# Kernel optimization log

Hardware: AMD Instinct MI355X
Metric: run time of the kernel (lower is better)

Reference implementation:

```python
import jax, jax.numpy as jnp
import numpy as np

N_HEAD = 12
EPS_NORM = 1e-12   # F.normalize eps
EPS_DENOM = 1e-6   # clamp(min=1e-6)


def _l2norm(t):
    n = jnp.sqrt(jnp.sum(t * t, axis=-1, keepdims=True))
    return t / jnp.maximum(n, EPS_NORM)


def setup_inputs() -> dict:
    key = jax.random.key(0)
    ks = jax.random.split(key, 5)
    B, T, C = 1, 4096, 768
    x = jax.random.normal(ks[0], (B, T, C), dtype=jnp.float32)
    w_attn = jax.random.normal(ks[1], (C, 3 * C), dtype=jnp.float32) * 0.02
    b_attn = jnp.zeros((3 * C,), dtype=jnp.float32)
    w_proj = jax.random.normal(ks[2], (C, C), dtype=jnp.float32) * 0.02
    b_proj = jnp.zeros((C,), dtype=jnp.float32)
    return {"x": x, "w_attn": w_attn, "b_attn": b_attn,
            "w_proj": w_proj, "b_proj": b_proj}


def reference(x, w_attn, b_attn, w_proj, b_proj):
    B, T, C = x.shape
    H = N_HEAD
    hd = C // H
    qkv = x @ w_attn + b_attn                      # [B,T,3C]
    q, k, v = jnp.split(qkv, 3, axis=-1)
    # [B,T,C] -> [B,H,T,hd]
    def to_heads(t):
        return t.reshape(B, T, H, hd).transpose(0, 2, 1, 3)
    q, k, v = to_heads(q), to_heads(k), to_heads(v)
    # T > 512 branch: normalized-qk cumulative linear attention
    q = _l2norm(q)
    k = _l2norm(k)
    num = jnp.einsum('bhqd,bhkd->bhqk', q, k)      # [B,H,T,T]
    denom = jnp.maximum(jnp.cumsum(num, axis=-1), EPS_DENOM)
    att = num / denom
    y = jnp.einsum('bhqk,bhkd->bhqd', att, v)      # [B,H,T,hd]
    y = y.transpose(0, 2, 1, 3).reshape(B, T, C)
    return y @ w_proj + b_proj
```

## Files before the change

kernel.cpp:

```cpp
#include <hip/hip_runtime.h>

#define T_SEQ 4096
#define H_NUM 12
#define HD    64
#define C_DIM 768
#define N_QKV 2304
#define HT    (T_SEQ * HD)
#define KT_TOT (T_SEQ / 64)

typedef float    f32x4 __attribute__((ext_vector_type(4)));
typedef float    f32x2 __attribute__((ext_vector_type(2)));
typedef _Float16 half8 __attribute__((ext_vector_type(8)));
typedef _Float16 half4 __attribute__((ext_vector_type(4)));
typedef _Float16 half2v __attribute__((ext_vector_type(2)));
typedef __fp16   fp16x2 __attribute__((ext_vector_type(2)));
typedef unsigned uint4v __attribute__((ext_vector_type(4)));

#define GLDS(gp, lp) __builtin_amdgcn_global_load_lds( \
    (const __attribute__((address_space(1))) void*)(gp), \
    (__attribute__((address_space(3))) void*)(lp), 16, 0, 0)

__device__ __forceinline__ void permlane32_swap(unsigned& a, unsigned& b) {
    asm("v_permlane32_swap_b32 %0, %1" : "+v"(a), "+v"(b));
}
__device__ __forceinline__ void permlane16_swap(unsigned& a, unsigned& b) {
    asm("v_permlane16_swap_b32 %0, %1" : "+v"(a), "+v"(b));
}

__global__ __launch_bounds__(256) void split_x_kernel(
    const float* __restrict__ x, _Float16* __restrict__ xh,
    _Float16* __restrict__ xl, int n4)
{
    const int i = blockIdx.x * 256 + threadIdx.x;
    if (i >= n4) return;
    const float4 v = ((const float4*)x)[i];
    const float vv[4] = {v.x, v.y, v.z, v.w};
    half4 h, l;
    #pragma unroll
    for (int j = 0; j < 4; ++j) {
        const _Float16 hh = (_Float16)vv[j];
        h[j] = hh;
        l[j] = (_Float16)(vv[j] - (float)hh);
    }
    ((half4*)xh)[i] = h;
    ((half4*)xl)[i] = l;
}

__global__ __launch_bounds__(256) void split_wt_kernel(
    const float* __restrict__ W, _Float16* __restrict__ wth,
    _Float16* __restrict__ wtl)
{
    __shared__ float Ws[64][65];
    const int tid = threadIdx.x;
    const int n0 = blockIdx.x * 64, k0 = blockIdx.y * 64;
    const int lr = tid >> 4, lc = (tid & 15) << 2;
    #pragma unroll
    for (int i = 0; i < 4; ++i) {
        const float4 v = *(const float4*)(W + (size_t)(k0 + lr + i * 16) * N_QKV + n0 + lc);
        Ws[lr + i * 16][lc + 0] = v.x; Ws[lr + i * 16][lc + 1] = v.y;
        Ws[lr + i * 16][lc + 2] = v.z; Ws[lr + i * 16][lc + 3] = v.w;
    }
    __syncthreads();
    const int n = tid >> 2, ks = (tid & 3) << 4;
    half8 h0, h1, l0, l1;
    #pragma unroll
    for (int j = 0; j < 8; ++j) {
        const float v = Ws[ks + j][n];
        const _Float16 hh = (_Float16)v;
        h0[j] = hh; l0[j] = (_Float16)(v - (float)hh);
    }
    #pragma unroll
    for (int j = 0; j < 8; ++j) {
        const float v = Ws[ks + 8 + j][n];
        const _Float16 hh = (_Float16)v;
        h1[j] = hh; l1[j] = (_Float16)(v - (float)hh);
    }
    const size_t dst = (size_t)(n0 + n) * C_DIM + k0 + ks;
    *(half8*)(wth + dst) = h0; *(half8*)(wth + dst + 8) = h1;
    *(half8*)(wtl + dst) = l0; *(half8*)(wtl + dst + 8) = l1;
}

__global__ __launch_bounds__(256) void gemm_qkv_kernel(
    const _Float16* __restrict__ xh, const _Float16* __restrict__ xl,
    const _Float16* __restrict__ wth, const _Float16* __restrict__ wtl,
    const float* __restrict__ bias,
    _Float16* __restrict__ qhi, _Float16* __restrict__ qlo,
    _Float16* __restrict__ khi, _Float16* __restrict__ klo,
    _Float16* __restrict__ vt)
{
    __shared__ __align__(16) _Float16 AH[128 * 64];
    __shared__ __align__(16) _Float16 AL[128 * 64];
    __shared__ __align__(16) _Float16 BH[64 * 64];
    __shared__ __align__(16) _Float16 BL[64 * 64];
    const int tid = threadIdx.x;
    const int wv = tid >> 6, lane = tid & 63;
    const int fm = lane & 15, fg = lane >> 4;
    const int lrow = lane >> 3;
    const int lcs  = (lane & 7) ^ (lrow & 7);
    const int bx = blockIdx.x;
    const int m0 = blockIdx.y * 128;

    auto dma_chunk = [&](int c) {
        const int kc0 = c * 64;
        #pragma unroll
        for (int i = 0; i < 12; ++i) {
            const int qidx = wv * 12 + i;
            if (qidx < 16) {
                const int rg = qidx;
                GLDS(xh + (size_t)(m0 + rg * 8 + lrow) * C_DIM + kc0 + lcs * 8, &AH[rg * 512]);
            } else if (qidx < 32) {
                const int rg = qidx - 16;
                GLDS(xl + (size_t)(m0 + rg * 8 + lrow) * C_DIM + kc0 + lcs * 8, &AL[rg * 512]);
            } else if (qidx < 40) {
                const int rg = qidx - 32;
                GLDS(wth + (size_t)(bx * 64 + rg * 8 + lrow) * C_DIM + kc0 + lcs * 8, &BH[rg * 512]);
            } else {
                const int rg = qidx - 40;
                GLDS(wtl + (size_t)(bx * 64 + rg * 8 + lrow) * C_DIM + kc0 + lcs * 8, &BL[rg * 512]);
            }
        }
    };

    f32x4 acc[2][4];
    #pragma unroll
    for (int mt = 0; mt < 2; ++mt)
        #pragma unroll
        for (int ct = 0; ct < 4; ++ct) acc[mt][ct] = (f32x4){0.f, 0.f, 0.f, 0.f};

    const int swz = fm & 7;
    dma_chunk(0);
    #pragma unroll 1
    for (int c = 0; c < C_DIM / 64; ++c) {
        __syncthreads();
        half8 ah[2][2], al[2][2], bh[4][2], bl[4][2];
        #pragma unroll
        for (int mt = 0; mt < 2; ++mt) {
            const int rb = (wv * 32 + mt * 16 + fm) * 64;
            #pragma unroll
            for (int kc = 0; kc < 2; ++kc) {
                const int cb = ((kc * 4 + fg) ^ swz) * 8;
                ah[mt][kc] = *(const half8*)&AH[rb + cb];
                al[mt][kc] = *(const half8*)&AL[rb + cb];
            }
        }
        #pragma unroll
        for (int ct = 0; ct < 4; ++ct) {
            const int rb = (ct * 16 + fm) * 64;
            #pragma unroll
            for (int kc = 0; kc < 2; ++kc) {
                const int cb = ((kc * 4 + fg) ^ swz) * 8;
                bh[ct][kc] = *(const half8*)&BH[rb + cb];
                bl[ct][kc] = *(const half8*)&BL[rb + cb];
            }
        }
        __syncthreads();
        if (c + 1 < C_DIM / 64) dma_chunk(c + 1);
        #pragma unroll
        for (int mt = 0; mt < 2; ++mt)
            #pragma unroll
            for (int ct = 0; ct < 4; ++ct)
                #pragma unroll
                for (int kc = 0; kc < 2; ++kc) {
                    acc[mt][ct] = __builtin_amdgcn_mfma_f32_16x16x32_f16(ah[mt][kc], bh[ct][kc], acc[mt][ct], 0, 0, 0);
                    acc[mt][ct] = __builtin_amdgcn_mfma_f32_16x16x32_f16(ah[mt][kc], bl[ct][kc], acc[mt][ct], 0, 0, 0);
                    acc[mt][ct] = __builtin_amdgcn_mfma_f32_16x16x32_f16(al[mt][kc], bh[ct][kc], acc[mt][ct], 0, 0, 0);
                }
    }

    const int sec = bx / 12, h = bx % 12;
    const size_t hb = (size_t)h * HT;
    float bb[4];
    #pragma unroll
    for (int ct = 0; ct < 4; ++ct) bb[ct] = bias[bx * 64 + ct * 16 + fm];

    if (sec < 2) {
        _Float16* dh = (sec == 0) ? qhi : khi;
        _Float16* dl = (sec == 0) ? qlo : klo;
        #pragma unroll
        for (int mt = 0; mt < 2; ++mt)
            #pragma unroll
            for (int r = 0; r < 4; ++r) {
                float o[4];
                float ss = 0.f;
                #pragma unroll
                for (int ct = 0; ct < 4; ++ct) {
                    o[ct] = acc[mt][ct][r] + bb[ct];
                    ss += o[ct] * o[ct];
                }
                #pragma unroll
                for (int mk = 1; mk < 16; mk <<= 1) ss += __shfl_xor(ss, mk, 16);
                const float invn = 1.0f / fmaxf(sqrtf(ss), 1e-12f);
                const int t = m0 + wv * 32 + mt * 16 + fg * 4 + r;
                const size_t rb = hb + (size_t)t * HD;
                #pragma unroll
                for (int ct = 0; ct < 4; ++ct) {
                    const float v = o[ct] * invn;
                    const _Float16 vh = (_Float16)v;
                    dh[rb + ct * 16 + fm] = vh;
                    dl[rb + ct * 16 + fm] = (_Float16)(v - (float)vh);
                }
            }
    } else {
        #pragma unroll
        for (int mt = 0; mt < 2; ++mt) {
            const int t0 = m0 + wv * 32 + mt * 16 + fg * 4;
            #pragma unroll
            for (int ct = 0; ct < 4; ++ct) {
                half4 pk;
                #pragma unroll
                for (int r = 0; r < 4; ++r) pk[r] = (_Float16)(acc[mt][ct][r] + bb[ct]);
                *(half4*)(vt + hb + (size_t)(ct * 16 + fm) * T_SEQ + t0) = pk;
            }
        }
    }
}

__global__ __launch_bounds__(256) void attn_kernel(
    const _Float16* __restrict__ qhi, const _Float16* __restrict__ qlo,
    const _Float16* __restrict__ khi, const _Float16* __restrict__ klo,
    const _Float16* __restrict__ vt,  _Float16* __restrict__ ylin)
{
    __shared__ __align__(16) _Float16 KH[2][64 * 64];
    __shared__ __align__(16) _Float16 KL[2][64 * 64];
    __shared__ __align__(16) _Float16 VS[2][64 * 64];

    const int tid = threadIdx.x;
    const int wv = tid >> 6, lane = tid & 63;
    const int fm = lane & 15, fg = lane >> 4;
    const int lrow = lane >> 3;
    const int lcs  = (lane & 7) ^ (lrow & 7);
    const int h = blockIdx.y, qt = blockIdx.x;
    const size_t hb = (size_t)h * HT;

    const int q = qt * 64 + wv * 16 + fm;
    half8 qf[2][2];
    #pragma unroll
    for (int kc = 0; kc < 2; ++kc) {
        const size_t off = hb + (size_t)q * HD + kc * 32 + fg * 8;
        qf[0][kc] = *(const half8*)(qhi + off);
        qf[1][kc] = *(const half8*)(qlo + off);
    }

    const _Float16* ga[6];
    _Float16*       lb[6];
    int             gstr[6];
    #pragma unroll
    for (int i = 0; i < 6; ++i) {
        const int qidx = wv * 6 + i;
        const int rg = qidx & 7;
        if (qidx < 8) {
            ga[i] = khi + hb + (size_t)(rg * 8 + lrow) * HD + lcs * 8;
            lb[i] = &KH[0][rg * 512];
            gstr[i] = 64 * HD;
        } else if (qidx < 16) {
            ga[i] = klo + hb + (size_t)(rg * 8 + lrow) * HD + lcs * 8;
            lb[i] = &KL[0][rg * 512];
            gstr[i] = 64 * HD;
        } else {
            ga[i] = vt + hb + (size_t)(rg * 8 + lrow) * T_SEQ + lcs * 8;
            lb[i] = &VS[0][rg * 512];
            gstr[i] = 64;
        }
    }
    auto issue_tiles = [&](int bufoff) {
        #pragma unroll
        for (int i = 0; i < 6; ++i) {
            GLDS(ga[i], lb[i] + bufoff);
            ga[i] += gstr[i];
        }
    };

    f32x4 yacc[4];
    #pragma unroll
    for (int ct = 0; ct < 4; ++ct) yacc[ct] = (f32x4){0.f, 0.f, 0.f, 0.f};
    float carry = 0.0f;
    const int swz = fm & 7;

    issue_tiles(0);
    #pragma unroll 1
    for (int kt = 0; kt < KT_TOT; ++kt) {
        const int cur = kt & 1;
        __syncthreads();
        if (kt + 1 < KT_TOT) issue_tiles((cur ^ 1) * 4096);

        half8 ka[4][2], kl[4][2], vf[4][2];
        #pragma unroll
        for (int kr = 0; kr < 4; ++kr) {
            const int rb = (kr * 16 + fm) * 64;
            #pragma unroll
            for (int kc = 0; kc < 2; ++kc) {
                const int cb = ((kc * 4 + fg) ^ swz) * 8;
                ka[kr][kc] = *(const half8*)&KH[cur][rb + cb];
                kl[kr][kc] = *(const half8*)&KL[cur][rb + cb];
            }
        }
        #pragma unroll
        for (int ct = 0; ct < 4; ++ct) {
            const int rb = (ct * 16 + fm) * 64;
            #pragma unroll
            for (int kc = 0; kc < 2; ++kc)
                vf[ct][kc] = *(const half8*)&VS[cur][rb + (((kc * 4 + fg) ^ swz) * 8)];
        }

        f32x4 sacc[4];
        #pragma unroll
        for (int kr = 0; kr < 4; ++kr) sacc[kr] = (f32x4){0.f, 0.f, 0.f, 0.f};
        #pragma unroll
        for (int kr = 0; kr < 4; ++kr)
            #pragma unroll
            for (int kc = 0; kc < 2; ++kc) {
                sacc[kr] = __builtin_amdgcn_mfma_f32_16x16x32_f16(ka[kr][kc], qf[0][kc], sacc[kr], 0, 0, 0);
                sacc[kr] = __builtin_amdgcn_mfma_f32_16x16x32_f16(ka[kr][kc], qf[1][kc], sacc[kr], 0, 0, 0);
                sacc[kr] = __builtin_amdgcn_mfma_f32_16x16x32_f16(kl[kr][kc], qf[0][kc], sacc[kr], 0, 0, 0);
            }

        unsigned pk[4][2];
        #pragma unroll
        for (int pr = 0; pr < 2; ++pr) {
            const int kra = 2 * pr, krb = 2 * pr + 1;
            const f32x2 S0 = {sacc[kra][0], sacc[krb][0]};
            const f32x2 S1 = {sacc[kra][1], sacc[krb][1]};
            const f32x2 S2 = {sacc[kra][2], sacc[krb][2]};
            const f32x2 S3 = {sacc[kra][3], sacc[krb][3]};
            const f32x2 P1 = S0 + S1;
            const f32x2 P2 = P1 + S2;
            const f32x2 P3 = P2 + S3;
            f32x2 U1;
            U1[0] = __shfl_xor(P3[0], 16, 64);
            U1[1] = __shfl_xor(P3[1], 16, 64);
            const f32x2 PAIR = P3 + U1;
            f32x2 U2;
            U2[0] = __shfl_xor(PAIR[0], 32, 64);
            U2[1] = __shfl_xor(PAIR[1], 32, 64);
            const f32x2 TOT = PAIR + U2;
            #pragma unroll
            for (int qq = 0; qq < 2; ++qq) {
                const int kr = 2 * pr + qq;
                const float pref = ((fg & 1) ? U1[qq] : 0.0f) + ((fg & 2) ? U2[qq] : 0.0f);
                const float base = carry + pref;
                carry += TOT[qq];
                const f32x2 b2 = {base, base};
                const f32x2 d01 = b2 + (f32x2){S0[qq], P1[qq]};
                const f32x2 d23 = b2 + (f32x2){P2[qq], P3[qq]};
                const f32x2 eps = {1e-6f, 1e-6f};
                const f32x2 m01 = __builtin_elementwise_max(d01, eps);
                const f32x2 m23 = __builtin_elementwise_max(d23, eps);
                const f32x2 r01 = {__builtin_amdgcn_rcpf(m01[0]), __builtin_amdgcn_rcpf(m01[1])};
                const f32x2 r23 = {__builtin_amdgcn_rcpf(m23[0]), __builtin_amdgcn_rcpf(m23[1])};
                const f32x2 n01 = {S0[qq], S1[qq]};
                const f32x2 n23 = {S2[qq], S3[qq]};
                const f32x2 sc = {0.03125f, 0.03125f};
                const f32x2 a01 = (n01 * r01) * sc;
                const f32x2 a23 = (n23 * r23) * sc;
                const fp16x2 c0 = __builtin_amdgcn_cvt_pkrtz(a01[0], a01[1]);
                const fp16x2 c1 = __builtin_amdgcn_cvt_pkrtz(a23[0], a23[1]);
                pk[kr][0] = __builtin_bit_cast(unsigned, c0);
                pk[kr][1] = __builtin_bit_cast(unsigned, c1);
            }
        }

        #pragma unroll
        for (int g = 0; g < 2; ++g)
            #pragma unroll
            for (int hh = 0; hh < 2; ++hh) {
                permlane32_swap(pk[g * 2 + 0][hh], pk[g * 2 + 1][hh]);
                permlane16_swap(pk[g * 2 + 0][hh], pk[g * 2 + 1][hh]);
            }

        #pragma unroll
        for (int kc = 0; kc < 2; ++kc) {
            const uint4v u = {pk[2 * kc][0], pk[2 * kc][1],
                              pk[2 * kc + 1][0], pk[2 * kc + 1][1]};
            const half8 af = __builtin_bit_cast(half8, u);
            #pragma unroll
            for (int ct = 0; ct < 4; ++ct)
                yacc[ct] = __builtin_amdgcn_mfma_f32_16x16x32_f16(af, vf[ct][kc], yacc[ct], 0, 0, 0);
        }
    }

    #pragma unroll
    for (int ct = 0; ct < 4; ++ct)
        #pragma unroll
        for (int r = 0; r < 4; ++r) {
            const int t = qt * 64 + wv * 16 + fg * 4 + r;
            ylin[(size_t)t * C_DIM + h * HD + ct * 16 + fm] =
                (_Float16)(yacc[ct][r] * 0.0078125f);
        }
}

__global__ __launch_bounds__(256) void gemm_proj_kernel(
    const _Float16* __restrict__ A, const float* __restrict__ W,
    const float* __restrict__ bias, float* __restrict__ out)
{
    __shared__ _Float16 As[64][72];
    __shared__ _Float16 Bt[64][72];
    const int tid = threadIdx.x;
    const int w = tid >> 6, lane = tid & 63;
    const int m = lane & 15, g = lane >> 4;
    const int row0 = blockIdx.x << 6, col0 = blockIdx.y << 6;
    const int ar = tid >> 3, ac8 = (tid & 7) << 3;
    const int bn0 = (tid & 15) << 2, bpv = tid >> 4;
    f32x4 acc[4];
    #pragma unroll
    for (int ct = 0; ct < 4; ++ct) acc[ct] = (f32x4){0.f, 0.f, 0.f, 0.f};

    for (int kt = 0; kt < C_DIM; kt += 64) {
        half8 av0 = *(const half8*)(A + (size_t)(row0 + ar)      * C_DIM + kt + ac8);
        half8 av1 = *(const half8*)(A + (size_t)(row0 + ar + 32) * C_DIM + kt + ac8);
        float4 w0[2], w1[2];
        #pragma unroll
        for (int i = 0; i < 2; ++i) {
            const int k = kt + 2 * (bpv + 16 * i);
            w0[i] = *(const float4*)(W + (size_t)k       * C_DIM + col0 + bn0);
            w1[i] = *(const float4*)(W + (size_t)(k + 1) * C_DIM + col0 + bn0);
        }
        __syncthreads();
        *(half8*)&As[ar][ac8]      = av0;
        *(half8*)&As[ar + 32][ac8] = av1;
        #pragma unroll
        for (int i = 0; i < 2; ++i) {
            const int p = bpv + 16 * i;
            const float a_[4] = {w0[i].x, w0[i].y, w0[i].z, w0[i].w};
            const float b_[4] = {w1[i].x, w1[i].y, w1[i].z, w1[i].w};
            #pragma unroll
            for (int u = 0; u < 4; ++u) {
                half2v pk = {(_Float16)a_[u], (_Float16)b_[u]};
                *(half2v*)&Bt[bn0 + u][2 * p] = pk;
            }
        }
        __syncthreads();
        #pragma unroll
        for (int kc = 0; kc < 2; ++kc) {
            const half8 a = *(half8*)&As[w * 16 + m][kc * 32 + g * 8];
            #pragma unroll
            for (int ct = 0; ct < 4; ++ct) {
                const half8 b = *(half8*)&Bt[ct * 16 + m][kc * 32 + g * 8];
                acc[ct] = __builtin_amdgcn_mfma_f32_16x16x32_f16(a, b, acc[ct], 0, 0, 0);
            }
        }
    }
    #pragma unroll
    for (int ct = 0; ct < 4; ++ct)
        #pragma unroll
        for (int r = 0; r < 4; ++r) {
            const int t = row0 + w * 16 + g * 4 + r;
            const int n = col0 + ct * 16 + m;
            out[(size_t)t * C_DIM + n] = acc[ct][r] * 4096.0f + bias[n];
        }
}

extern "C" void kernel_launch(void* const* d_in, const int* in_sizes, int n_in,
                              void* d_out, int out_size, void* d_ws, size_t ws_size,
                              hipStream_t stream)
{
    const float* x      = (const float*)d_in[0];
    const float* w_attn = (const float*)d_in[1];
    const float* b_attn = (const float*)d_in[2];
    const float* w_proj = (const float*)d_in[3];
    const float* b_proj = (const float*)d_in[4];
    float* out = (float*)d_out;

    const size_t perQK = (size_t)H_NUM * HT;
    const size_t perX  = (size_t)T_SEQ * C_DIM;
    const size_t perW  = (size_t)N_QKV * C_DIM;
    _Float16* base = (_Float16*)d_ws;
    _Float16* xhi  = base;
    _Float16* xlo  = xhi + perX;
    _Float16* wthi = xlo + perX;
    _Float16* wtlo = wthi + perW;
    _Float16* qhi  = wtlo + perW;
    _Float16* qlo  = qhi + perQK;
    _Float16* khi  = qlo + perQK;
    _Float16* klo  = khi + perQK;
    _Float16* vtp  = klo + perQK;
    _Float16* ylin = xhi;

    split_x_kernel<<<(perX / 4 + 255) / 256, 256, 0, stream>>>(x, xhi, xlo, perX / 4);
    split_wt_kernel<<<dim3(N_QKV / 64, C_DIM / 64), 256, 0, stream>>>(w_attn, wthi, wtlo);
    gemm_qkv_kernel<<<dim3(N_QKV / 64, T_SEQ / 128), 256, 0, stream>>>(
        xhi, xlo, wthi, wtlo, b_attn, qhi, qlo, khi, klo, vtp);
    attn_kernel<<<dim3(T_SEQ / 64, H_NUM), 256, 0, stream>>>(
        qhi, qlo, khi, klo, vtp, ylin);
    gemm_proj_kernel<<<dim3(T_SEQ / 64, C_DIM / 64), 256, 0, stream>>>(
        ylin, w_proj, b_proj, out);
}
```

Measured before the change: 302.2 us.

## Software-pipeline QK^T of next tile with scan and PV of current tile

After: 321.0 us. 6.2% more time.

```diff
diff --git a/kernel.cpp b/kernel.cpp
--- a/kernel.cpp
+++ b/kernel.cpp
@@ -276,52 +276,49 @@
     float carry = 0.0f;
     const int swz = fm & 7;
 
-    issue_tiles(0);
-    #pragma unroll 1
-    for (int kt = 0; kt < KT_TOT; ++kt) {
-        const int cur = kt & 1;
-        __syncthreads();
-        if (kt + 1 < KT_TOT) issue_tiles((cur ^ 1) * 4096);
-
-        half8 ka[4][2], kl[4][2], vf[4][2];
+    f32x4 saccA[4], saccB[4];
+    half8 vfA[4][2], vfB[4][2];
+
+    auto qkt = [&](int nb, f32x4 (&sn)[4]) {
         #pragma unroll
         for (int kr = 0; kr < 4; ++kr) {
             const int rb = (kr * 16 + fm) * 64;
-            #pragma unroll
-            for (int kc = 0; kc < 2; ++kc) {
-                const int cb = ((kc * 4 + fg) ^ swz) * 8;
-                ka[kr][kc] = *(const half8*)&KH[cur][rb + cb];
-                kl[kr][kc] = *(const half8*)&KL[cur][rb + cb];
-            }
-        }
+            const int cb0 = (fg ^ swz) * 8;
+            const int cb1 = ((4 + fg) ^ swz) * 8;
+            const half8 a0 = *(const half8*)&KH[nb][rb + cb0];
+            const half8 a1 = *(const half8*)&KH[nb][rb + cb1];
+            const half8 l0 = *(const half8*)&KL[nb][rb + cb0];
+            const half8 l1 = *(const half8*)&KL[nb][rb + cb1];
+            f32x4 s = (f32x4){0.f, 0.f, 0.f, 0.f};
+            s = __builtin_amdgcn_mfma_f32_16x16x32_f16(a0, qf[0][0], s, 0, 0, 0);
+            s = __builtin_amdgcn_mfma_f32_16x16x32_f16(a0, qf[1][0], s, 0, 0, 0);
+            s = __builtin_amdgcn_mfma_f32_16x16x32_f16(l0, qf[0][0], s, 0, 0, 0);
+            s = __builtin_amdgcn_mfma_f32_16x16x32_f16(a1, qf[0][1], s, 0, 0, 0);
+            s = __builtin_amdgcn_mfma_f32_16x16x32_f16(a1, qf[1][1], s, 0, 0, 0);
+            s = __builtin_amdgcn_mfma_f32_16x16x32_f16(l1, qf[0][1], s, 0, 0, 0);
+            sn[kr] = s;
+        }
+    };
+
+    auto rdv = [&](int nb, half8 (&v)[4][2]) {
         #pragma unroll
         for (int ct = 0; ct < 4; ++ct) {
             const int rb = (ct * 16 + fm) * 64;
             #pragma unroll
             for (int kc = 0; kc < 2; ++kc)
-                vf[ct][kc] = *(const half8*)&VS[cur][rb + (((kc * 4 + fg) ^ swz) * 8)];
-        }
-
-        f32x4 sacc[4];
-        #pragma unroll
-        for (int kr = 0; kr < 4; ++kr) sacc[kr] = (f32x4){0.f, 0.f, 0.f, 0.f};
-        #pragma unroll
-        for (int kr = 0; kr < 4; ++kr)
-            #pragma unroll
-            for (int kc = 0; kc < 2; ++kc) {
-                sacc[kr] = __builtin_amdgcn_mfma_f32_16x16x32_f16(ka[kr][kc], qf[0][kc], sacc[kr], 0, 0, 0);
-                sacc[kr] = __builtin_amdgcn_mfma_f32_16x16x32_f16(ka[kr][kc], qf[1][kc], sacc[kr], 0, 0, 0);
-                sacc[kr] = __builtin_amdgcn_mfma_f32_16x16x32_f16(kl[kr][kc], qf[0][kc], sacc[kr], 0, 0, 0);
-            }
-
+                v[ct][kc] = *(const half8*)&VS[nb][rb + (((kc * 4 + fg) ^ swz) * 8)];
+        }
+    };
+
+    auto scanpv = [&](f32x4 (&s)[4], half8 (&v)[4][2]) {
         unsigned pk[4][2];
         #pragma unroll
         for (int pr = 0; pr < 2; ++pr) {
             const int kra = 2 * pr, krb = 2 * pr + 1;
-            const f32x2 S0 = {sacc[kra][0], sacc[krb][0]};
-            const f32x2 S1 = {sacc[kra][1], sacc[krb][1]};
-            const f32x2 S2 = {sacc[kra][2], sacc[krb][2]};
-            const f32x2 S3 = {sacc[kra][3], sacc[krb][3]};
+            const f32x2 S0 = {s[kra][0], s[krb][0]};
+            const f32x2 S1 = {s[kra][1], s[krb][1]};
+            const f32x2 S2 = {s[kra][2], s[krb][2]};
+            const f32x2 S3 = {s[kra][3], s[krb][3]};
             const f32x2 P1 = S0 + S1;
             const f32x2 P2 = P1 + S2;
             const f32x2 P3 = P2 + S3;
@@ -358,7 +355,6 @@
                 pk[kr][1] = __builtin_bit_cast(unsigned, c1);
             }
         }
-
         #pragma unroll
         for (int g = 0; g < 2; ++g)
             #pragma unroll
@@ -366,7 +362,6 @@
                 permlane32_swap(pk[g * 2 + 0][hh], pk[g * 2 + 1][hh]);
                 permlane16_swap(pk[g * 2 + 0][hh], pk[g * 2 + 1][hh]);
             }
-
         #pragma unroll
         for (int kc = 0; kc < 2; ++kc) {
             const uint4v u = {pk[2 * kc][0], pk[2 * kc][1],
@@ -374,9 +369,34 @@
             const half8 af = __builtin_bit_cast(half8, u);
             #pragma unroll
             for (int ct = 0; ct < 4; ++ct)
-                yacc[ct] = __builtin_amdgcn_mfma_f32_16x16x32_f16(af, vf[ct][kc], yacc[ct], 0, 0, 0);
-        }
-    }
+                yacc[ct] = __builtin_amdgcn_mfma_f32_16x16x32_f16(af, v[ct][kc], yacc[ct], 0, 0, 0);
+        }
+    };
+
+    auto step = [&](int nb, f32x4 (&sc)[4], f32x4 (&sn)[4],
+                    half8 (&vc)[4][2], half8 (&vn)[4][2], bool dodma) {
+        __syncthreads();
+        rdv(nb, vn);
+        if (dodma) issue_tiles((nb ^ 1) * 4096);
+        qkt(nb, sn);
+        scanpv(sc, vc);
+    };
+
+    issue_tiles(0);
+    issue_tiles(4096);
+    __syncthreads();
+    rdv(0, vfA);
+    qkt(0, saccA);
+
+    step(1, saccA, saccB, vfA, vfB, true);
+    #pragma unroll 1
+    for (int j = 0; j < 30; ++j) {
+        step(0, saccB, saccA, vfB, vfA, true);
+        step(1, saccA, saccB, vfA, vfB, true);
+    }
+    step(0, saccB, saccA, vfB, vfA, true);
+    step(1, saccA, saccB, vfA, vfB, false);
+    scanpv(saccB, vfB);
 
     #pragma unroll
     for (int ct = 0; ct < 4; ++ct)
```

## Pre-transpose proj weights to fp16 and stream proj GEMM tiles via async LDS loads

Applied to the files above, without the earlier changes.

After: 315.5 us. 1.04x slower.

```diff
diff --git a/kernel.cpp b/kernel.cpp
--- a/kernel.cpp
+++ b/kernel.cpp
@@ -78,6 +78,30 @@
     const size_t dst = (size_t)(n0 + n) * C_DIM + k0 + ks;
     *(half8*)(wth + dst) = h0; *(half8*)(wth + dst + 8) = h1;
     *(half8*)(wtl + dst) = l0; *(half8*)(wtl + dst + 8) = l1;
+}
+
+__global__ __launch_bounds__(256) void split_wp_kernel(
+    const float* __restrict__ W, _Float16* __restrict__ wpt)
+{
+    __shared__ float Ws[64][65];
+    const int tid = threadIdx.x;
+    const int n0 = blockIdx.x * 64, k0 = blockIdx.y * 64;
+    const int lr = tid >> 4, lc = (tid & 15) << 2;
+    #pragma unroll
+    for (int i = 0; i < 4; ++i) {
+        const float4 v = *(const float4*)(W + (size_t)(k0 + lr + i * 16) * C_DIM + n0 + lc);
+        Ws[lr + i * 16][lc + 0] = v.x; Ws[lr + i * 16][lc + 1] = v.y;
+        Ws[lr + i * 16][lc + 2] = v.z; Ws[lr + i * 16][lc + 3] = v.w;
+    }
+    __syncthreads();
+    const int n = tid >> 2, ks = (tid & 3) << 4;
+    half8 h0, h1;
+    #pragma unroll
+    for (int j = 0; j < 8; ++j) h0[j] = (_Float16)Ws[ks + j][n];
+    #pragma unroll
+    for (int j = 0; j < 8; ++j) h1[j] = (_Float16)Ws[ks + 8 + j][n];
+    const size_t dst = (size_t)(n0 + n) * C_DIM + k0 + ks;
+    *(half8*)(wpt + dst) = h0; *(half8*)(wpt + dst + 8) = h1;
 }
 
 __global__ __launch_bounds__(256) void gemm_qkv_kernel(
@@ -389,62 +413,70 @@
 }
 
 __global__ __launch_bounds__(256) void gemm_proj_kernel(
-    const _Float16* __restrict__ A, const float* __restrict__ W,
+    const _Float16* __restrict__ A, const _Float16* __restrict__ wpt,
     const float* __restrict__ bias, float* __restrict__ out)
 {
-    __shared__ _Float16 As[64][72];
-    __shared__ _Float16 Bt[64][72];
+    __shared__ __align__(16) _Float16 AS[64 * 64];
+    __shared__ __align__(16) _Float16 BS[64 * 64];
     const int tid = threadIdx.x;
-    const int w = tid >> 6, lane = tid & 63;
-    const int m = lane & 15, g = lane >> 4;
-    const int row0 = blockIdx.x << 6, col0 = blockIdx.y << 6;
-    const int ar = tid >> 3, ac8 = (tid & 7) << 3;
-    const int bn0 = (tid & 15) << 2, bpv = tid >> 4;
+    const int wv = tid >> 6, lane = tid & 63;
+    const int fm = lane & 15, fg = lane >> 4;
+    const int lrow = lane >> 3;
+    const int lcs  = (lane & 7) ^ (lrow & 7);
+    const int m0 = blockIdx.x * 64, n0 = blockIdx.y * 64;
+
+    auto dma_chunk = [&](int c) {
+        const int kc0 = c * 64;
+        #pragma unroll
+        for (int i = 0; i < 4; ++i) {
+            const int qidx = wv * 4 + i;
+            if (qidx < 8) {
+                const int rg = qidx;
+                GLDS(A + (size_t)(m0 + rg * 8 + lrow) * C_DIM + kc0 + lcs * 8, &AS[rg * 512]);
+            } else {
+                const int rg = qidx - 8;
+                GLDS(wpt + (size_t)(n0 + rg * 8 + lrow) * C_DIM + kc0 + lcs * 8, &BS[rg * 512]);
+            }
+        }
+    };
+
     f32x4 acc[4];
     #pragma unroll
     for (int ct = 0; ct < 4; ++ct) acc[ct] = (f32x4){0.f, 0.f, 0.f, 0.f};
 
-    for (int kt = 0; kt < C_DIM; kt += 64) {
-        half8 av0 = *(const half8*)(A + (size_t)(row0 + ar)      * C_DIM + kt + ac8);
-        half8 av1 = *(const half8*)(A + (size_t)(row0 + ar + 32) * C_DIM + kt + ac8);
-        float4 w0[2], w1[2];
-        #pragma unroll
-        for (int i = 0; i < 2; ++i) {
-            const int k = kt + 2 * (bpv + 16 * i);
-            w0[i] = *(const float4*)(W + (size_t)k       * C_DIM + col0 + bn0);
-            w1[i] = *(const float4*)(W + (size_t)(k + 1) * C_DIM + col0 + bn0);
-        }
+    const int swz = fm & 7;
+    dma_chunk(0);
+    #pragma unroll 1
+    for (int c = 0; c < C_DIM / 64; ++c) {
         __syncthreads();
-        *(half8*)&As[ar][ac8]      = av0;
-        *(half8*)&As[ar + 32][ac8] = av1;
-        #pragma unroll
-        for (int i = 0; i < 2; ++i) {
-            const int p = bpv + 16 * i;
-            const float a_[4] = {w0[i].x, w0[i].y, w0[i].z, w0[i].w};
-            const float b_[4] = {w1[i].x, w1[i].y, w1[i].z, w1[i].w};
-            #pragma unroll
-            for (int u = 0; u < 4; ++u) {
-                half2v pk = {(_Float16)a_[u], (_Float16)b_[u]};
-                *(half2v*)&Bt[bn0 + u][2 * p] = pk;
-            }
+        half8 a[2], b[4][2];
+        {
+            const int rb = (wv * 16 + fm) * 64;
+            #pragma unroll
+            for (int kc = 0; kc < 2; ++kc)
+                a[kc] = *(const half8*)&AS[rb + (((kc * 4 + fg) ^ swz) * 8)];
+        }
+        #pragma unroll
+        for (int ct = 0; ct < 4; ++ct) {
+            const int rb = (ct * 16 + fm) * 64;
+            #pragma unroll
+            for (int kc = 0; kc < 2; ++kc)
+                b[ct][kc] = *(const half8*)&BS[rb + (((kc * 4 + fg) ^ swz) * 8)];
         }
         __syncthreads();
-        #pragma unroll
-        for (int kc = 0; kc < 2; ++kc) {
-            const half8 a = *(half8*)&As[w * 16 + m][kc * 32 + g * 8];
-            #pragma unroll
-            for (int ct = 0; ct < 4; ++ct) {
-                const half8 b = *(half8*)&Bt[ct * 16 + m][kc * 32 + g * 8];
-                acc[ct] = __builtin_amdgcn_mfma_f32_16x16x32_f16(a, b, acc[ct], 0, 0, 0);
-            }
-        }
+        if (c + 1 < C_DIM / 64) dma_chunk(c + 1);
+        #pragma unroll
+        for (int kc = 0; kc < 2; ++kc)
+            #pragma unroll
+            for (int ct = 0; ct < 4; ++ct)
+                acc[ct] = __builtin_amdgcn_mfma_f32_16x16x32_f16(a[kc], b[ct][kc], acc[ct], 0, 0, 0);
     }
     #pragma unroll
     for (int ct = 0; ct < 4; ++ct)
         #pragma unroll
         for (int r = 0; r < 4; ++r) {
-            const int t = row0 + w * 16 + g * 4 + r;
-            const int n = col0 + ct * 16 + m;
+            const int t = m0 + wv * 16 + fg * 4 + r;
+            const int n = n0 + ct * 16 + fm;
             out[(size_t)t * C_DIM + n] = acc[ct][r] * 4096.0f + bias[n];
         }
 }
@@ -474,13 +506,15 @@
     _Float16* klo  = khi + perQK;
     _Float16* vtp  = klo + perQK;
     _Float16* ylin = xhi;
+    _Float16* wpt  = wtlo;
 
     split_x_kernel<<<(perX / 4 + 255) / 256, 256, 0, stream>>>(x, xhi, xlo, perX / 4);
     split_wt_kernel<<<dim3(N_QKV / 64, C_DIM / 64), 256, 0, stream>>>(w_attn, wthi, wtlo);
     gemm_qkv_kernel<<<dim3(N_QKV / 64, T_SEQ / 128), 256, 0, stream>>>(
         xhi, xlo, wthi, wtlo, b_attn, qhi, qlo, khi, klo, vtp);
+    split_wp_kernel<<<dim3(C_DIM / 64, C_DIM / 64), 256, 0, stream>>>(w_proj, wpt);
     attn_kernel<<<dim3(T_SEQ / 64, H_NUM), 256, 0, stream>>>(
         qhi, qlo, khi, klo, vtp, ylin);
     gemm_proj_kernel<<<dim3(T_SEQ / 64, C_DIM / 64), 256, 0, stream>>>(
-        ylin, w_proj, b_proj, out);
-}
+        ylin, wpt, b_proj, out);
+}
```
